# Kernel optimization log

Hardware: AMD Instinct MI355X
Metric: run time of the kernel (lower is better)

The kernel has to match this reference:

```python
import jax, jax.numpy as jnp
import numpy as np

B, H, LK, D = 8, 16, 4096, 128


def setup_inputs() -> dict:
    key = jax.random.key(0)
    ks = jax.random.split(key, 9)
    s = 1.0 / np.sqrt(D)
    return {
        "Q": jax.random.normal(ks[0], (B, H, 1, D), dtype=jnp.float32),
        "K": jax.random.normal(ks[1], (B, H, LK, D), dtype=jnp.float32),
        "V": jax.random.normal(ks[2], (B, H, LK, D), dtype=jnp.float32),
        "mask": jax.random.randint(ks[3], (B, H, 1, LK), 0, 2, dtype=jnp.int32),
        "scale": 1,  # accepted but unused by the original forward
        "W_pre": jax.random.normal(ks[4], (D, D), dtype=jnp.float32) * s,
        "b_pre": jax.random.normal(ks[5], (D,), dtype=jnp.float32) * s,
        "W_q": jax.random.normal(ks[6], (D, D), dtype=jnp.float32) * s,
        "W_v": jax.random.normal(ks[7], (D, 1), dtype=jnp.float32) * s,
    }


def reference(Q, K, V, mask, scale, W_pre, b_pre, W_q, W_v):
    # precompute = linear_pre(K): [B,H,LK,D]
    pre = jnp.einsum("bhkd,de->bhke", K, W_pre) + b_pre
    # targetT = linear_q(Q): [B,H,1,D], broadcast-added over keys
    tq = jnp.einsum("bhqd,de->bhqe", Q, W_q)
    tmp = jnp.tanh(pre + tq)  # [B,H,LK,D]
    # energy = linear_v(tmp) reshaped to [B,H,1,LK]
    energy = jnp.einsum("bhkd,d->bhk", tmp, W_v[:, 0])[:, :, None, :]
    m = mask.astype(energy.dtype)
    energy = energy * (1.0 - m) + m * (-1e6)
    score = jax.nn.softmax(energy, axis=-1)  # [B,H,1,LK]
    context = jnp.matmul(score, V)  # [B,H,1,D]
    return (context, score, pre)
```

## Files before the change

### kernel.cpp

```cpp
#include <hip/hip_runtime.h>
#include <hip/hip_bf16.h>
#include <math.h>

#define B_   8
#define H_   16
#define BH_  (B_*H_)
#define LK_  4096
#define D_   128

#define SEG   16
#define KSEG  (LK_/SEG)

typedef __attribute__((ext_vector_type(8))) short bf16x8;
typedef __attribute__((ext_vector_type(4))) float f32x4;
typedef __attribute__((ext_vector_type(4))) unsigned int u32x4;

__device__ __forceinline__ float fast_tanh(float x) {
    float ax = fabsf(x);
    float e  = __expf(2.0f * ax);
    float r  = 1.0f - __fdividef(2.0f, e + 1.0f);
    return copysignf(r, x);
}

__device__ __forceinline__ unsigned int cvtpk(float lo, float hi) {
    unsigned int r;
    asm("v_cvt_pk_bf16_f32 %0, %1, %2" : "=v"(r) : "v"(lo), "v"(hi));
    return r;
}

__device__ __forceinline__ unsigned short cvt_hi(float x) {
    __hip_bfloat16 bh = __float2bfloat16(x);
    return __builtin_bit_cast(unsigned short, bh);
}

__device__ __forceinline__ void cvt8v(const f32x4 a, const f32x4 b, bf16x8& h, bf16x8& l) {
    unsigned int h0 = cvtpk(a[0], a[1]);
    unsigned int h1 = cvtpk(a[2], a[3]);
    unsigned int h2 = cvtpk(b[0], b[1]);
    unsigned int h3 = cvtpk(b[2], b[3]);
    float l0 = a[0] - __uint_as_float(h0 << 16);
    float l1 = a[1] - __uint_as_float(h0 & 0xFFFF0000u);
    float l2 = a[2] - __uint_as_float(h1 << 16);
    float l3 = a[3] - __uint_as_float(h1 & 0xFFFF0000u);
    float l4 = b[0] - __uint_as_float(h2 << 16);
    float l5 = b[1] - __uint_as_float(h2 & 0xFFFF0000u);
    float l6 = b[2] - __uint_as_float(h3 << 16);
    float l7 = b[3] - __uint_as_float(h3 & 0xFFFF0000u);
    u32x4 hv = {h0, h1, h2, h3};
    u32x4 lv = {cvtpk(l0, l1), cvtpk(l2, l3), cvtpk(l4, l5), cvtpk(l6, l7)};
    h = __builtin_bit_cast(bf16x8, hv);
    l = __builtin_bit_cast(bf16x8, lv);
}

__device__ __forceinline__ void gld_lds16(const void* g, void* l) {
    __builtin_amdgcn_global_load_lds(
        (const __attribute__((address_space(1))) unsigned int*)g,
        (__attribute__((address_space(3))) unsigned int*)l,
        16, 0, 0);
}

__global__ void pack_kernel(const float* __restrict__ Wpre,
                            unsigned short* __restrict__ Whi) {
    int idx  = blockIdx.x * 256 + threadIdx.x;
    int j    = idx & 7;
    int lane = (idx >> 3) & 63;
    int nt   = (idx >> 9) & 7;
    int ks   = idx >> 12;
    int k    = ks * 32 + (lane >> 4) * 8 + j;
    int n    = nt * 16 + (lane & 15);
    Whi[idx] = cvt_hi(Wpre[k * D_ + n]);
}

__global__ void tq_kernel(const float* __restrict__ Q,
                          const float* __restrict__ Wq,
                          float* __restrict__ tq) {
    int bh = blockIdx.x;
    int e  = threadIdx.x;
    const float* q = Q + bh * D_;
    float acc = 0.0f;
#pragma unroll 8
    for (int d = 0; d < D_; ++d)
        acc = fmaf(q[d], Wq[d * D_ + e], acc);
    tq[bh * D_ + e] = acc;
}

__global__ void __launch_bounds__(256, 3)
main_kernel(const float* __restrict__ K,
            const unsigned short* __restrict__ Whi,
            const float* __restrict__ bpre,
            const float* __restrict__ Wv,
            const float* __restrict__ tqg,
            float* __restrict__ pre_out,
            float* __restrict__ ep0,
            float* __restrict__ ep1) {
    const int t    = threadIdx.x;
    const int lane = t & 63;
    const int wv_  = t >> 6;
    const int kg   = wv_ & 1;
    const int eh   = wv_ >> 1;
    const int l15  = lane & 15;
    const int lg   = lane >> 4;
    const int bh   = blockIdx.y;
    const int kblk = blockIdx.x * 256;

    __shared__ float Klds[3][4096];

    const float* Kbh = K + (size_t)bh * LK_ * D_;

    bf16x8 wf[4][4];
#pragma unroll
    for (int ks = 0; ks < 4; ++ks)
#pragma unroll
        for (int et = 0; et < 4; ++et)
            wf[ks][et] = *(const bf16x8*)(Whi + (((size_t)ks * 8 + eh * 4 + et) * 64 + lane) * 8);

    float4 bpv[4], tqv[4], wvv[4];
#pragma unroll
    for (int et = 0; et < 4; ++et) {
        const int e0 = eh * 64 + et * 16 + lg * 4;
        bpv[et] = *(const float4*)(bpre + e0);
        tqv[et] = *(const float4*)(tqg + bh * D_ + e0);
        wvv[et] = *(const float4*)(Wv + e0);
    }

    float* epo = (eh == 0) ? ep0 : ep1;

    auto stageK = [&](int s, int buf) {
#pragma unroll
        for (int i = 0; i < 4; ++i) {
            const int g4  = wv_ * 4 + i;
            const int kg2 = g4 >> 3, ks2 = (g4 >> 1) & 3, h2 = g4 & 1;
            const int row = kblk + s * 32 + kg2 * 16 + l15;
            const int col = lg * 8 + ks2 * 32 + h2 * 4;
            gld_lds16(Kbh + (size_t)row * D_ + col, &Klds[buf][g4 * 256]);
        }
    };

    stageK(0, 0);
    stageK(1, 1);
    asm volatile("s_waitcnt vmcnt(4)\n\ts_barrier" ::: "memory");

#pragma unroll
    for (int s = 0; s < 8; ++s) {
        if (s + 2 < 8) stageK(s + 2, (s + 2) % 3);

        const float* kb = Klds[s % 3];
        f32x4 acc[4];
#pragma unroll
        for (int et = 0; et < 4; ++et)
            acc[et] = (f32x4){0.f, 0.f, 0.f, 0.f};

#pragma unroll
        for (int ks = 0; ks < 4; ++ks) {
            const int gbase = ((kg * 4 + ks) * 2) * 256 + lane * 4;
            f32x4 p0 = *(const f32x4*)(kb + gbase);
            f32x4 p1 = *(const f32x4*)(kb + gbase + 256);
            bf16x8 kh, kl;
            cvt8v(p0, p1, kh, kl);
#pragma unroll
            for (int et = 0; et < 4; ++et) {
                acc[et] = __builtin_amdgcn_mfma_f32_16x16x32_bf16(wf[ks][et], kh, acc[et], 0, 0, 0);
                acc[et] = __builtin_amdgcn_mfma_f32_16x16x32_bf16(wf[ks][et], kl, acc[et], 0, 0, 0);
            }
        }

        const int key = kblk + s * 32 + kg * 16 + l15;
        float* pb = pre_out + (size_t)bh * LK_ * D_ + (size_t)key * D_;
        float ep = 0.0f;
#pragma unroll
        for (int et = 0; et < 4; ++et) {
            const int e0 = eh * 64 + et * 16 + lg * 4;
            f32x4 a = acc[et];
            f32x4 v;
            v[0] = a[0] + bpv[et].x;
            v[1] = a[1] + bpv[et].y;
            v[2] = a[2] + bpv[et].z;
            v[3] = a[3] + bpv[et].w;
            __builtin_nontemporal_store(v, (f32x4*)(pb + e0));
            ep = fmaf(fast_tanh(v[0] + tqv[et].x), wvv[et].x, ep);
            ep = fmaf(fast_tanh(v[1] + tqv[et].y), wvv[et].y, ep);
            ep = fmaf(fast_tanh(v[2] + tqv[et].z), wvv[et].z, ep);
            ep = fmaf(fast_tanh(v[3] + tqv[et].w), wvv[et].w, ep);
        }
        ep += __shfl_xor(ep, 16, 64);
        ep += __shfl_xor(ep, 32, 64);
        epo[(size_t)bh * LK_ + key] = ep;

        if (s == 0)
            asm volatile("s_waitcnt vmcnt(9)\n\ts_barrier" ::: "memory");
        else if (s < 6)
            asm volatile("s_waitcnt vmcnt(14)\n\ts_barrier" ::: "memory");
        else if (s == 6)
            asm volatile("s_waitcnt vmcnt(10)\n\ts_barrier" ::: "memory");
    }
}

__global__ void ml_kernel(const float* __restrict__ ep0,
                          const float* __restrict__ ep1,
                          const int* __restrict__ mask,
                          float* __restrict__ ml) {
    const int bh = blockIdx.x;
    const int t  = threadIdx.x;
    const float* e0 = ep0 + (size_t)bh * LK_;
    const float* e1 = ep1 + (size_t)bh * LK_;
    const int*   m  = mask + (size_t)bh * LK_;

    float mx = -1e30f;
    for (int k = t; k < LK_; k += 256) {
        float v = m[k] ? -1.0e6f : (e0[k] + e1[k]);
        mx = fmaxf(mx, v);
    }
#pragma unroll
    for (int off = 32; off > 0; off >>= 1)
        mx = fmaxf(mx, __shfl_xor(mx, off, 64));
    __shared__ float wmax[4];
    if ((t & 63) == 0) wmax[t >> 6] = mx;
    __syncthreads();
    mx = fmaxf(fmaxf(wmax[0], wmax[1]), fmaxf(wmax[2], wmax[3]));

    float sum = 0.0f;
    for (int k = t; k < LK_; k += 256) {
        float v = m[k] ? -1.0e6f : (e0[k] + e1[k]);
        sum += __expf(v - mx);
    }
#pragma unroll
    for (int off = 32; off > 0; off >>= 1)
        sum += __shfl_xor(sum, off, 64);
    __shared__ float wsum[4];
    if ((t & 63) == 0) wsum[t >> 6] = sum;
    __syncthreads();
    if (t == 0) {
        ml[bh * 2]     = mx;
        ml[bh * 2 + 1] = wsum[0] + wsum[1] + wsum[2] + wsum[3];
    }
}

__global__ void score_ctx_kernel(const float* __restrict__ ep1,
                                 const int* __restrict__ mask,
                                 const float* __restrict__ V,
                                 const float* __restrict__ ml,
                                 float* __restrict__ score_out,
                                 float* __restrict__ part) {
    const int seg = blockIdx.x;
    const int bh  = blockIdx.y;
    const int t   = threadIdx.x;
    const int k0  = seg * KSEG;

    __shared__ float sc[KSEG];
    __shared__ float pl[8][136];

    const float mx  = ml[bh * 2];
    const float inv = 1.0f / ml[bh * 2 + 1];

    {
        const size_t gi = (size_t)bh * LK_ + k0 + t;
        float v = mask[gi] ? -1.0e6f : (score_out[gi] + ep1[gi]);
        float s = __expf(v - mx) * inv;
        sc[t] = s;
        score_out[gi] = s;
    }
    __syncthreads();

    const int d4 = t & 31;
    const int g  = t >> 5;
    const float* Vb = V + ((size_t)bh * LK_ + k0) * D_ + d4 * 4;
    float4 a = make_float4(0.f, 0.f, 0.f, 0.f);
#pragma unroll 4
    for (int kk = g; kk < KSEG; kk += 8) {
        float4 vv = *(const float4*)(Vb + (size_t)kk * D_);
        float s = sc[kk];
        a.x = fmaf(s, vv.x, a.x);
        a.y = fmaf(s, vv.y, a.y);
        a.z = fmaf(s, vv.z, a.z);
        a.w = fmaf(s, vv.w, a.w);
    }
    *(float4*)&pl[g][d4 * 4] = a;
    __syncthreads();

    if (t < 128) {
        float s = 0.0f;
#pragma unroll
        for (int gg = 0; gg < 8; ++gg)
            s += pl[gg][t];
        part[((size_t)bh * SEG + seg) * D_ + t] = s;
    }
}

__global__ void combine_kernel(const float* __restrict__ part,
                               float* __restrict__ ctx) {
    const int bh = blockIdx.x;
    const int d  = threadIdx.x;
    float s = 0.0f;
#pragma unroll
    for (int g = 0; g < SEG; ++g)
        s += part[((size_t)bh * SEG + g) * D_ + d];
    ctx[bh * D_ + d] = s;
}

extern "C" void kernel_launch(void* const* d_in, const int* in_sizes, int n_in,
                              void* d_out, int out_size, void* d_ws, size_t ws_size,
                              hipStream_t stream) {
    const float* Q    = (const float*)d_in[0];
    const float* K    = (const float*)d_in[1];
    const float* V    = (const float*)d_in[2];
    const int*   mask = (const int*)  d_in[3];
    const float* Wpre = (const float*)d_in[5];
    const float* bpre = (const float*)d_in[6];
    const float* Wq   = (const float*)d_in[7];
    const float* Wv   = (const float*)d_in[8];

    float* out   = (float*)d_out;
    float* ctx   = out;
    float* score = out + (size_t)BH_ * D_;
    float* pre   = score + (size_t)BH_ * LK_;

    float* w    = (float*)d_ws;
    float* tq   = w;
    float* ml   = tq + (size_t)BH_ * D_;
    float* part = ml + 2 * BH_;
    unsigned short* Whi = (unsigned short*)(part + (size_t)BH_ * SEG * D_);
    float* ep1  = (float*)(Whi + 16384);

    hipLaunchKernelGGL(pack_kernel, dim3(64), dim3(256), 0, stream, Wpre, Whi);
    hipLaunchKernelGGL(tq_kernel, dim3(BH_), dim3(D_), 0, stream, Q, Wq, tq);
    hipLaunchKernelGGL(main_kernel, dim3(LK_ / 256, BH_), dim3(256), 0, stream,
                       K, Whi, bpre, Wv, tq, pre, score, ep1);
    hipLaunchKernelGGL(ml_kernel, dim3(BH_), dim3(256), 0, stream, score, ep1, mask, ml);
    hipLaunchKernelGGL(score_ctx_kernel, dim3(SEG, BH_), dim3(256), 0, stream,
                       ep1, mask, V, ml, score, part);
    hipLaunchKernelGGL(combine_kernel, dim3(BH_), dim3(D_), 0, stream, part, ctx);
}
```

Baseline: 202.5 us.

## Stage K via registers into padded LDS instead of direct global-to-LDS loads

Replaces the global_load_lds direct-to-LDS staging of K with coalesced row-wise register loads that are written into a padded (132-float stride) double-buffered LDS tile. Fragment reads then come from the row-major padded layout, which is meant to improve global coalescing and avoid LDS bank conflicts. In exchange it uses more VGPRs for two register staging buffers and adds explicit LDS writes and lgkmcnt waits each step. The triple-buffered LDS becomes double-buffered, with the vmcnt counts hand-tuned to match.

```diff
diff --git a/kernel.cpp b/kernel.cpp
--- a/kernel.cpp
+++ b/kernel.cpp
@@ -10,6 +10,8 @@
 
 #define SEG   16
 #define KSEG  (LK_/SEG)
+
+#define LROW 132
 
 typedef __attribute__((ext_vector_type(8))) short bf16x8;
 typedef __attribute__((ext_vector_type(4))) float f32x4;
@@ -50,13 +52,6 @@
     u32x4 lv = {cvtpk(l0, l1), cvtpk(l2, l3), cvtpk(l4, l5), cvtpk(l6, l7)};
     h = __builtin_bit_cast(bf16x8, hv);
     l = __builtin_bit_cast(bf16x8, lv);
-}
-
-__device__ __forceinline__ void gld_lds16(const void* g, void* l) {
-    __builtin_amdgcn_global_load_lds(
-        (const __attribute__((address_space(1))) unsigned int*)g,
-        (__attribute__((address_space(3))) unsigned int*)l,
-        16, 0, 0);
 }
 
 __global__ void pack_kernel(const float* __restrict__ Wpre,
@@ -103,7 +98,7 @@
     const int bh   = blockIdx.y;
     const int kblk = blockIdx.x * 256;
 
-    __shared__ float Klds[3][4096];
+    __shared__ float Klds[2][32 * LROW];
 
     const float* Kbh = K + (size_t)bh * LK_ * D_;
 
@@ -125,26 +120,39 @@
 
     float* epo = (eh == 0) ? ep0 : ep1;
 
-    auto stageK = [&](int s, int buf) {
-#pragma unroll
-        for (int i = 0; i < 4; ++i) {
-            const int g4  = wv_ * 4 + i;
-            const int kg2 = g4 >> 3, ks2 = (g4 >> 1) & 3, h2 = g4 & 1;
-            const int row = kblk + s * 32 + kg2 * 16 + l15;
-            const int col = lg * 8 + ks2 * 32 + h2 * 4;
-            gld_lds16(Kbh + (size_t)row * D_ + col, &Klds[buf][g4 * 256]);
+    const int srow[4] = { (0 * 256 + t) >> 5, (1 * 256 + t) >> 5,
+                          (2 * 256 + t) >> 5, (3 * 256 + t) >> 5 };
+    const int sc4 = t & 31;
+
+    f32x4 rA[4], rB[4];
+
+    auto loadK = [&](int s, f32x4* r) {
+#pragma unroll
+        for (int i = 0; i < 4; ++i)
+            r[i] = *(const f32x4*)(Kbh + (size_t)(kblk + s * 32 + srow[i]) * D_ + sc4 * 4);
+    };
+    auto writeK = [&](int buf, const f32x4* r) {
+#pragma unroll
+        for (int i = 0; i < 4; ++i)
+            *(f32x4*)(&Klds[buf][srow[i] * LROW + sc4 * 4]) = r[i];
+    };
+
+    loadK(0, rA);
+    loadK(1, rB);
+    asm volatile("s_waitcnt vmcnt(4)" ::: "memory");
+    writeK(0, rA);
+    asm volatile("s_waitcnt lgkmcnt(0)\n\ts_barrier" ::: "memory");
+
+    const int rbase = (kg * 16 + l15) * LROW + lg * 8;
+
+#pragma unroll
+    for (int s = 0; s < 8; ++s) {
+        if (s + 2 < 8) {
+            if ((s & 1) == 0) loadK(s + 2, rA);
+            else              loadK(s + 2, rB);
         }
-    };
-
-    stageK(0, 0);
-    stageK(1, 1);
-    asm volatile("s_waitcnt vmcnt(4)\n\ts_barrier" ::: "memory");
-
-#pragma unroll
-    for (int s = 0; s < 8; ++s) {
-        if (s + 2 < 8) stageK(s + 2, (s + 2) % 3);
-
-        const float* kb = Klds[s % 3];
+
+        const float* kb = Klds[s & 1];
         f32x4 acc[4];
 #pragma unroll
         for (int et = 0; et < 4; ++et)
@@ -152,9 +160,8 @@
 
 #pragma unroll
         for (int ks = 0; ks < 4; ++ks) {
-            const int gbase = ((kg * 4 + ks) * 2) * 256 + lane * 4;
-            f32x4 p0 = *(const f32x4*)(kb + gbase);
-            f32x4 p1 = *(const f32x4*)(kb + gbase + 256);
+            f32x4 p0 = *(const f32x4*)(kb + rbase + ks * 32);
+            f32x4 p1 = *(const f32x4*)(kb + rbase + ks * 32 + 4);
             bf16x8 kh, kl;
             cvt8v(p0, p1, kh, kl);
 #pragma unroll
@@ -186,12 +193,17 @@
         ep += __shfl_xor(ep, 32, 64);
         epo[(size_t)bh * LK_ + key] = ep;
 
-        if (s == 0)
-            asm volatile("s_waitcnt vmcnt(9)\n\ts_barrier" ::: "memory");
-        else if (s < 6)
-            asm volatile("s_waitcnt vmcnt(14)\n\ts_barrier" ::: "memory");
-        else if (s == 6)
-            asm volatile("s_waitcnt vmcnt(10)\n\ts_barrier" ::: "memory");
+        if (s + 1 < 8) {
+            if (s == 0)
+                asm volatile("s_waitcnt vmcnt(9)" ::: "memory");
+            else if (s < 6)
+                asm volatile("s_waitcnt vmcnt(14)" ::: "memory");
+            else
+                asm volatile("s_waitcnt vmcnt(10)" ::: "memory");
+            if ((s & 1) == 0) writeK(1, rB);
+            else              writeK(0, rA);
+            asm volatile("s_waitcnt lgkmcnt(0)\n\ts_barrier" ::: "memory");
+        }
     }
 }
 
```

Result: slower. 291.1 us (+43.8%).
